# Kernel tuning notes

Hardware: AMD Instinct MI355X
Metric: run time of the kernel (lower is better)

The kernel has to match this reference:

```python
import jax, jax.numpy as jnp
import numpy as np


def setup_inputs() -> dict:
    key = jax.random.key(0)
    B, C, H, W = 16, 3, 512, 512
    num_bins = 8
    # Bin geometry exactly as in HistLayer.__init__
    bin_edges = np.linspace(-0.05, 1.05, num_bins + 1)
    half_width = (bin_edges[2] - bin_edges[1]) / 2.0
    centers = (bin_edges + half_width)[:-1]  # [num_bins]
    return {
        "input_image": jax.random.uniform(key, (B, C, H, W), dtype=jnp.float32),
        "centers": jnp.asarray(centers, dtype=jnp.float32),   # bin_centers_conv bias = -centers
        "width": jnp.float32(half_width),                      # bin_widths_conv bias
    }


def reference(input_image, centers, width):
    """Differentiable hard-binning histogram (fused form of the grouped 1x1 convs).

    bin_centers_conv (weight=1, bias=-c) -> x - c, broadcast over num_bins
    abs
    bin_widths_conv (weight=-1, bias=w) -> w - |x - c|
    1.01 ** z, then Threshold(1, 0): keep values > 1 else 0
    two_d: flatten spatial; one_d: global average pool (normalize=True path).
    """
    B, C, H, W = input_image.shape
    NB = centers.shape[0]
    # [B, C, NB, H, W]: per-channel broadcast against every bin center
    z = width - jnp.abs(input_image[:, :, None, :, :] - centers[None, None, :, None, None])
    p = jnp.power(jnp.asarray(1.01, input_image.dtype), z)
    xx = jnp.where(p > 1, p, jnp.zeros((), input_image.dtype))
    xx = xx.reshape(B, C * NB, H * W)
    two_d = xx
    one_d = xx.mean(axis=2)  # AdaptiveAvgPool2d(1) then flatten
    return one_d, two_d
```

## Files before the change

kernel.cpp:

```cpp
#include <hip/hip_runtime.h>
#include <math.h>

namespace {
constexpr int NBINS = 8;
constexpr int HW4 = (512 * 512) / 4;
constexpr int PLANES = 16 * 3;
constexpr double LN_BASE = 0.0099503214108481;
constexpr double KEEP_THRESH = 1.0 + 1.0 / 16777216.0;
constexpr float LOG2_BASE = 0.014355293f;

typedef float v4f __attribute__((ext_vector_type(4)));

__device__ __forceinline__ float binval(float z) {
  if (!(z > 0.0f)) return 0.0f;
  if (z < 1.0e-5f) {
    double p = exp((double)z * LN_BASE);
    if (!(p > KEEP_THRESH)) return 0.0f;
  }
  return exp2f(z * LOG2_BASE);
}
}

__global__ __launch_bounds__(256) void hist_kernel(
    const float4* __restrict__ in, const float* __restrict__ centers,
    const float* __restrict__ wptr, float* __restrict__ out) {
  const int plane = blockIdx.y;
  const int i4 = blockIdx.x * 256 + threadIdx.x;
  const float w = wptr[0];
  float c[NBINS];
#pragma unroll
  for (int k = 0; k < NBINS; ++k) c[k] = centers[k];

  const float4 x = in[(size_t)plane * HW4 + i4];
  v4f* const out2 = reinterpret_cast<v4f*>(out + PLANES * NBINS) +
                    (size_t)plane * NBINS * HW4 + i4;
  float sums[NBINS];
#pragma unroll
  for (int k = 0; k < NBINS; ++k) {
    v4f v;
    v.x = binval(w - fabsf(x.x - c[k]));
    v.y = binval(w - fabsf(x.y - c[k]));
    v.z = binval(w - fabsf(x.z - c[k]));
    v.w = binval(w - fabsf(x.w - c[k]));
    __builtin_nontemporal_store(v, out2 + (size_t)k * HW4);
    sums[k] = (v.x + v.y) + (v.z + v.w);
  }

#pragma unroll
  for (int k = 0; k < NBINS; ++k) {
#pragma unroll
    for (int off = 32; off > 0; off >>= 1)
      sums[k] += __shfl_down(sums[k], off, 64);
  }
  __shared__ float part[4][NBINS];
  const int lane = threadIdx.x & 63;
  const int wv = threadIdx.x >> 6;
  if (lane == 0) {
#pragma unroll
    for (int k = 0; k < NBINS; ++k) part[wv][k] = sums[k];
  }
  __syncthreads();
  if (threadIdx.x < NBINS) {
    float s = (part[0][threadIdx.x] + part[1][threadIdx.x]) +
              (part[2][threadIdx.x] + part[3][threadIdx.x]);
    atomicAdd(out + plane * NBINS + threadIdx.x, s * (1.0f / 262144.0f));
  }
}

extern "C" void kernel_launch(void* const* d_in, const int* in_sizes, int n_in,
                              void* d_out, int out_size, void* d_ws, size_t ws_size,
                              hipStream_t stream) {
  const float4* in = (const float4*)d_in[0];
  const float* centers = (const float*)d_in[1];
  const float* width = (const float*)d_in[2];
  float* out = (float*)d_out;
  (void)hipMemsetAsync(d_out, 0, PLANES * NBINS * sizeof(float), stream);
  hist_kernel<<<dim3(256, PLANES), 256, 0, stream>>>(in, centers, width, out);
}
```

Measured before the change: 430.7 us.

## Replace double-precision threshold test with float cutoff and transpose-style shuffle reduction

Replaces the per-element branch with a double-precision exp by a single float comparison against a precomputed cutoff Tf, the largest float whose exponent still gives a power above 1. The 8 per-bin wave reductions (48 shuffles) become a butterfly exchange that halves the bins at each step, so each lane ends up with one bin's sum. The input load is made nontemporal and the output stores are moved after the reduction. This removes divergent double-precision work and shuffle overhead in a kernel that is mostly bound by store bandwidth, and it holds all 8 result vectors in registers until the end.

```diff
diff --git a/kernel.cpp b/kernel.cpp
--- a/kernel.cpp
+++ b/kernel.cpp
@@ -5,72 +5,96 @@
 constexpr int NBINS = 8;
 constexpr int HW4 = (512 * 512) / 4;
 constexpr int PLANES = 16 * 3;
-constexpr double LN_BASE = 0.0099503214108481;
-constexpr double KEEP_THRESH = 1.0 + 1.0 / 16777216.0;
+constexpr double LN_BASE = 0.00995032141084807;
+constexpr double LOG1P_EPS = 5.960464299903379e-8;
 constexpr float LOG2_BASE = 0.014355293f;
 
 typedef float v4f __attribute__((ext_vector_type(4)));
-
-__device__ __forceinline__ float binval(float z) {
-  if (!(z > 0.0f)) return 0.0f;
-  if (z < 1.0e-5f) {
-    double p = exp((double)z * LN_BASE);
-    if (!(p > KEEP_THRESH)) return 0.0f;
-  }
-  return exp2f(z * LOG2_BASE);
-}
 }
 
 __global__ __launch_bounds__(256) void hist_kernel(
-    const float4* __restrict__ in, const float* __restrict__ centers,
+    const v4f* __restrict__ in, const float* __restrict__ centers,
     const float* __restrict__ wptr, float* __restrict__ out) {
   const int plane = blockIdx.y;
   const int i4 = blockIdx.x * 256 + threadIdx.x;
   const float w = wptr[0];
+
+  const double T = LOG1P_EPS / LN_BASE;
+  float Tf = (float)T;
+  if ((double)Tf >= T) Tf = __builtin_nextafterf(Tf, 0.0f);
+
   float c[NBINS];
 #pragma unroll
   for (int k = 0; k < NBINS; ++k) c[k] = centers[k];
 
-  const float4 x = in[(size_t)plane * HW4 + i4];
-  v4f* const out2 = reinterpret_cast<v4f*>(out + PLANES * NBINS) +
-                    (size_t)plane * NBINS * HW4 + i4;
-  float sums[NBINS];
+  const v4f x = __builtin_nontemporal_load(in + (size_t)plane * HW4 + i4);
+
+  v4f vv[NBINS];
+  float s[NBINS];
 #pragma unroll
   for (int k = 0; k < NBINS; ++k) {
     v4f v;
-    v.x = binval(w - fabsf(x.x - c[k]));
-    v.y = binval(w - fabsf(x.y - c[k]));
-    v.z = binval(w - fabsf(x.z - c[k]));
-    v.w = binval(w - fabsf(x.w - c[k]));
-    __builtin_nontemporal_store(v, out2 + (size_t)k * HW4);
-    sums[k] = (v.x + v.y) + (v.z + v.w);
+    {
+      float z = w - fabsf(x.x - c[k]);
+      v.x = (z > Tf) ? exp2f(z * LOG2_BASE) : 0.0f;
+      z = w - fabsf(x.y - c[k]);
+      v.y = (z > Tf) ? exp2f(z * LOG2_BASE) : 0.0f;
+      z = w - fabsf(x.z - c[k]);
+      v.z = (z > Tf) ? exp2f(z * LOG2_BASE) : 0.0f;
+      z = w - fabsf(x.w - c[k]);
+      v.w = (z > Tf) ? exp2f(z * LOG2_BASE) : 0.0f;
+    }
+    vv[k] = v;
+    s[k] = (v.x + v.y) + (v.z + v.w);
   }
 
+  const int lane = threadIdx.x & 63;
+  const int h1 = lane & 1;
+  float t[4];
 #pragma unroll
-  for (int k = 0; k < NBINS; ++k) {
+  for (int k = 0; k < 4; ++k) {
+    float keep = h1 ? s[k + 4] : s[k];
+    float send = h1 ? s[k] : s[k + 4];
+    t[k] = keep + __shfl_xor(send, 1, 64);
+  }
+  const int h2 = (lane >> 1) & 1;
+  float u[2];
 #pragma unroll
-    for (int off = 32; off > 0; off >>= 1)
-      sums[k] += __shfl_down(sums[k], off, 64);
+  for (int k = 0; k < 2; ++k) {
+    float keep = h2 ? t[k + 2] : t[k];
+    float send = h2 ? t[k] : t[k + 2];
+    u[k] = keep + __shfl_xor(send, 2, 64);
   }
-  __shared__ float part[4][NBINS];
-  const int lane = threadIdx.x & 63;
-  const int wv = threadIdx.x >> 6;
-  if (lane == 0) {
+  const int h3 = (lane >> 2) & 1;
+  {
+    float keep = h3 ? u[1] : u[0];
+    float send = h3 ? u[0] : u[1];
+    float v0 = keep + __shfl_xor(send, 4, 64);
+    v0 += __shfl_xor(v0, 8, 64);
+    v0 += __shfl_xor(v0, 16, 64);
+    v0 += __shfl_xor(v0, 32, 64);
+    __shared__ float part[4][NBINS];
+    const int wv = threadIdx.x >> 6;
+    if (lane < NBINS) part[wv][4 * h1 + 2 * h2 + h3] = v0;
+    __syncthreads();
+    if (threadIdx.x < NBINS) {
+      float s8 = (part[0][threadIdx.x] + part[1][threadIdx.x]) +
+                 (part[2][threadIdx.x] + part[3][threadIdx.x]);
+      atomicAdd(out + plane * NBINS + threadIdx.x, s8 * (1.0f / 262144.0f));
+    }
+  }
+
+  v4f* const out2 = reinterpret_cast<v4f*>(out + PLANES * NBINS) +
+                    (size_t)plane * NBINS * HW4 + i4;
 #pragma unroll
-    for (int k = 0; k < NBINS; ++k) part[wv][k] = sums[k];
-  }
-  __syncthreads();
-  if (threadIdx.x < NBINS) {
-    float s = (part[0][threadIdx.x] + part[1][threadIdx.x]) +
-              (part[2][threadIdx.x] + part[3][threadIdx.x]);
-    atomicAdd(out + plane * NBINS + threadIdx.x, s * (1.0f / 262144.0f));
-  }
+  for (int k = 0; k < NBINS; ++k)
+    __builtin_nontemporal_store(vv[k], out2 + (size_t)k * HW4);
 }
 
 extern "C" void kernel_launch(void* const* d_in, const int* in_sizes, int n_in,
                               void* d_out, int out_size, void* d_ws, size_t ws_size,
                               hipStream_t stream) {
-  const float4* in = (const float4*)d_in[0];
+  const v4f* in = (const v4f*)d_in[0];
   const float* centers = (const float*)d_in[1];
   const float* width = (const float*)d_in[2];
   float* out = (float*)d_out;
```

Result: no change. 433.4 us (+0.6%).
